# Kernel optimization log

Hardware: AMD Instinct MI355X
Metric: run time of the kernel (lower is better)

The kernel has to match this reference:

```python
import jax, jax.numpy as jnp
import numpy as np

E = 64          # num_experts
D_IN = 512      # in_features
D_OUT = 512     # out_features
T = 262144      # total routed token-slots (grouped by expert, balanced)


def setup_inputs() -> dict:
    key = jax.random.key(0)
    k1, k2 = jax.random.split(key)
    STD = 0.02
    return {
        "input": jax.random.normal(k1, (T, D_IN), dtype=jnp.float32),
        # tokens are pre-grouped by expert; balanced routing -> equal counts
        "num_experts_per_token": jnp.full((E,), T // E, dtype=jnp.int64),
        "weight": jax.random.normal(k2, (E, D_OUT, D_IN), dtype=jnp.float32) * STD,
        "bias": jnp.zeros((E, D_OUT), dtype=jnp.float32),
    }


def reference(input, num_experts_per_token, weight, bias):
    # Faithful to the split + per-expert F.linear + cat path, for balanced
    # routing (equal counts per expert) so shapes are static under jit.
    e = weight.shape[0]
    tpe = input.shape[0] // e  # tokens per expert
    x = input.reshape(e, tpe, -1)                      # [E, tpe, D_in]
    # F.linear(x_e, W_e) = x_e @ W_e.T for each expert -> grouped GEMM
    out = jnp.einsum('eti,eoi->eto', x, weight)        # [E, tpe, D_out]
    out = out + bias[:, None, :]
    return out.reshape(e * tpe, -1)                    # [T, D_out]
```

## Files before the change

### kernel.cpp

```cpp
#include <hip/hip_runtime.h>
#include <hip/hip_bf16.h>


#define NEXPERT 64
#define DIN 512
#define DOUT 512
#define TPE 4096
#define BM 256
#define BN 256
#define BK 64
#define NKT 8

typedef __attribute__((ext_vector_type(8))) __bf16 bf16x8;
typedef __attribute__((ext_vector_type(4))) float f32x4;

__global__ __launch_bounds__(256)
void pack_w_kernel(const float* __restrict__ w, __bf16* __restrict__ wp) {
  int S = blockIdx.x * 256 + threadIdx.x;
  int l  = S & 63;
  int j  = (S >> 6) & 31;
  int kt = (S >> 11) & 7;
  int nt = (S >> 14) & 1;
  int e  = S >> 15;
  int o  = nt * 256 + j * 8 + (l >> 3);
  int kc = (l & 7) ^ (l >> 3);
  const float* src = w + ((size_t)(e * DOUT + o)) * DIN + kt * BK + kc * 8;
  f32x4 lo = *(const f32x4*)(src);
  f32x4 hi = *(const f32x4*)(src + 4);
  bf16x8 r;
  r[0]=(__bf16)lo[0]; r[1]=(__bf16)lo[1]; r[2]=(__bf16)lo[2]; r[3]=(__bf16)lo[3];
  r[4]=(__bf16)hi[0]; r[5]=(__bf16)hi[1]; r[6]=(__bf16)hi[2]; r[7]=(__bf16)hi[3];
  *(bf16x8*)(wp + (size_t)S * 8) = r;
}

__global__ __launch_bounds__(512, 2)
void moe_gemm256(const float* __restrict__ x, const __bf16* __restrict__ wp,
                 const float* __restrict__ bias, float* __restrict__ out) {
  __shared__ __align__(16) unsigned char sA[2][BM * BK * 2];
  __shared__ __align__(16) unsigned char sB[2][BN * BK * 2];

  int bid  = blockIdx.x;
  int swzb = (bid & 7) * 256 + (bid >> 3);
  int e  = swzb >> 5;
  int rr = swzb & 31;
  int mt = rr >> 1;
  int nt = rr & 1;

  const int tid  = threadIdx.x;
  const int lane = tid & 63;
  const int wv   = tid >> 6;
  const int wm   = wv >> 2;
  const int wn   = wv & 3;
  const int r15  = lane & 15;
  const int kg   = lane >> 4;

  const int xt0 = ((kg)     ^ (r15 & 7)) << 4;
  const int xt1 = ((4 + kg) ^ (r15 & 7)) << 4;
  const int aRdBase = (wm * 128 + r15) * 128;
  const int bRdBase = (wn * 64  + r15) * 128;

  const int ar = tid >> 1;
  const int h  = tid & 1;
  const float* aG = x + ((size_t)e * TPE + (size_t)mt * BM + ar) * DIN + h * 32;
  const int awr0 = ar * 128;

  const __bf16* bS0 = wp + (size_t)(e * 2 + nt) * 131072
                         + (size_t)(wv * 4) * 512 + (size_t)lane * 8;

  f32x4 sa[8];

#define GLOADB(kt, dbuf)                                                     \
  { _Pragma("unroll") for (int i = 0; i < 4; ++i)                            \
      __builtin_amdgcn_global_load_lds(                                      \
          (const __attribute__((address_space(1))) void*)(bS0 +              \
              (size_t)(kt) * 16384 + i * 512),                               \
          (__attribute__((address_space(3))) void*)(&sB[dbuf][(wv * 4 + i) * 1024]), \
          16, 0, 0); }

#define ISSUEA(kt)                                                           \
  { _Pragma("unroll") for (int i = 0; i < 8; ++i)                            \
      sa[i] = *(const f32x4*)(aG + (kt) * BK + i * 4); }

#define WRITEA(dbuf)                                                         \
  { _Pragma("unroll") for (int i2 = 0; i2 < 4; ++i2) {                       \
      bf16x8 cc;                                                             \
      cc[0]=(__bf16)sa[i2*2][0];   cc[1]=(__bf16)sa[i2*2][1];                \
      cc[2]=(__bf16)sa[i2*2][2];   cc[3]=(__bf16)sa[i2*2][3];                \
      cc[4]=(__bf16)sa[i2*2+1][0]; cc[5]=(__bf16)sa[i2*2+1][1];              \
      cc[6]=(__bf16)sa[i2*2+1][2]; cc[7]=(__bf16)sa[i2*2+1][3];              \
      *(bf16x8*)(&sA[dbuf][awr0 + (((h*4+i2) ^ (ar & 7)) << 4)]) = cc; } }

#define READB(d)                                                             \
  { _Pragma("unroll") for (int ni = 0; ni < 4; ++ni) {                       \
      bfr[ni][0] = *(const bf16x8*)(&sB[d][bRdBase + ni*2048 + xt0]);        \
      bfr[ni][1] = *(const bf16x8*)(&sB[d][bRdBase + ni*2048 + xt1]); } }

#define READA(p, d, af)                                                      \
  { _Pragma("unroll") for (int mi = 0; mi < 2; ++mi) {                       \
      af[mi][0] = *(const bf16x8*)(&sA[d][aRdBase + (p)*4096 + mi*2048 + xt0]); \
      af[mi][1] = *(const bf16x8*)(&sA[d][aRdBase + (p)*4096 + mi*2048 + xt1]); } }

#define MFMAP(p, af)                                                         \
  { __builtin_amdgcn_s_setprio(1);                                           \
    _Pragma("unroll") for (int mi = 0; mi < 2; ++mi)                         \
      _Pragma("unroll") for (int ni = 0; ni < 4; ++ni)                       \
        _Pragma("unroll") for (int kk = 0; kk < 2; ++kk)                     \
          acc[(p)*2+mi][ni] = __builtin_amdgcn_mfma_f32_16x16x32_bf16(       \
              af[mi][kk], bfr[ni][kk], acc[(p)*2+mi][ni], 0, 0, 0);          \
    __builtin_amdgcn_s_setprio(0); }

  f32x4 acc[8][4];
#pragma unroll
  for (int m = 0; m < 8; ++m)
#pragma unroll
    for (int n = 0; n < 4; ++n) acc[m][n] = (f32x4)0.f;

  GLOADB(0, 0);
  ISSUEA(0);
  WRITEA(0);
  asm volatile("s_waitcnt lgkmcnt(0)" ::: "memory");
  __builtin_amdgcn_s_barrier();

  bf16x8 bfr[4][2];

#pragma unroll
  for (int t = 0; t < NKT - 1; ++t) {
    const int d = t & 1;
    GLOADB(t + 1, d ^ 1);
    ISSUEA(t + 1);
    READB(d);
    bf16x8 af0[2][2], af1[2][2], af2[2][2], af3[2][2];
    READA(0, d, af0);
    MFMAP(0, af0);
    READA(1, d, af1);
    MFMAP(1, af1);
    READA(2, d, af2);
    MFMAP(2, af2);
    READA(3, d, af3);
    WRITEA(d ^ 1);
    MFMAP(3, af3);
    asm volatile("s_waitcnt lgkmcnt(0)" ::: "memory");
    __builtin_amdgcn_s_barrier();
  }

  {
    const int d = 1;
    READB(d);
    bf16x8 af[2][2];
    READA(0, d, af); MFMAP(0, af);
    READA(1, d, af); MFMAP(1, af);
    READA(2, d, af); MFMAP(2, af);
    READA(3, d, af); MFMAP(3, af);
  }

  float bv[4];
  const float* bp = bias + (size_t)e * DOUT + nt * BN + wn * 64 + r15;
#pragma unroll
  for (int n = 0; n < 4; ++n) bv[n] = bp[n * 16];

  const int q4 = (lane >> 4) * 4;
  float* Cb = out + ((size_t)e * TPE + (size_t)mt * BM + wm * 128) * DOUT
              + nt * BN + wn * 64;
#pragma unroll
  for (int m = 0; m < 8; ++m) {
#pragma unroll
    for (int j = 0; j < 4; ++j) {
      float* pr = Cb + (size_t)(m * 16 + q4 + j) * DOUT;
#pragma unroll
      for (int n = 0; n < 4; ++n)
        pr[n * 16 + r15] = acc[m][n][j] + bv[n];
    }
  }
#undef GLOADB
#undef ISSUEA
#undef WRITEA
#undef READB
#undef READA
#undef MFMAP
}

__device__ __forceinline__ bf16x8 cvt8f(f32x4 lo, f32x4 hi) {
  bf16x8 r;
  r[0]=(__bf16)lo[0]; r[1]=(__bf16)lo[1]; r[2]=(__bf16)lo[2]; r[3]=(__bf16)lo[3];
  r[4]=(__bf16)hi[0]; r[5]=(__bf16)hi[1]; r[6]=(__bf16)hi[2]; r[7]=(__bf16)hi[3];
  return r;
}

__global__ __launch_bounds__(256)
void moe_fallback(const float* __restrict__ x, const float* __restrict__ w,
                  const float* __restrict__ bias, float* __restrict__ out) {
  __shared__ bf16x8 fA[2][512];
  __shared__ bf16x8 fB[2][512];
  int bid = blockIdx.x;
  int swz = (bid & 7) * 1024 + (bid >> 3);
  int e = swz >> 7, rr = swz & 127, mt = rr >> 2, nt = rr & 3;
  const int t = threadIdx.x, lane = t & 63, wave = t >> 6;
  const int wm = wave >> 1, wnn = wave & 1, r15 = lane & 15, kgf = lane >> 4;
  const int rs = r15 * 4 + (kgf ^ ((r15 >> 1) & 3));
  const int row0 = t >> 2, kg0 = t & 3;
  const int slot0 = row0 * 4 + (kg0 ^ ((row0 >> 1) & 3));
  const int slot1 = slot0 + 256;
  const float* Ab = x + ((size_t)e * TPE + (size_t)mt * 128) * DIN;
  const float* Bb = w + ((size_t)e * DOUT + (size_t)nt * 128) * DIN;
  const int offA0 = row0 * DIN + kg0 * 8, offA1 = offA0 + 64 * DIN;
  f32x4 a0l, a0h, a1l, a1h, b0l, b0h, b1l, b1h;
  auto LOAD = [&](int kt) {
    const float* pa0 = Ab + offA0 + kt * 32; const float* pa1 = Ab + offA1 + kt * 32;
    const float* pb0 = Bb + offA0 + kt * 32; const float* pb1 = Bb + offA1 + kt * 32;
    a0l = *(const f32x4*)(pa0); a0h = *(const f32x4*)(pa0 + 4);
    a1l = *(const f32x4*)(pa1); a1h = *(const f32x4*)(pa1 + 4);
    b0l = *(const f32x4*)(pb0); b0h = *(const f32x4*)(pb0 + 4);
    b1l = *(const f32x4*)(pb1); b1h = *(const f32x4*)(pb1 + 4);
  };
  auto STORE = [&](int buf) {
    fA[buf][slot0] = cvt8f(a0l, a0h); fA[buf][slot1] = cvt8f(a1l, a1h);
    fB[buf][slot0] = cvt8f(b0l, b0h); fB[buf][slot1] = cvt8f(b1l, b1h);
  };
  f32x4 acc[4][4];
#pragma unroll
  for (int m = 0; m < 4; ++m)
#pragma unroll
    for (int n = 0; n < 4; ++n) acc[m][n] = (f32x4)0.f;
  LOAD(0); STORE(0); __syncthreads();
  int cur = 0;
  for (int kt = 0; kt < 16; ++kt) {
    if (kt + 1 < 16) LOAD(kt + 1);
    bf16x8 af[4], bfr[4];
#pragma unroll
    for (int m = 0; m < 4; ++m) af[m] = fA[cur][wm * 256 + m * 64 + rs];
#pragma unroll
    for (int n = 0; n < 4; ++n) bfr[n] = fB[cur][wnn * 256 + n * 64 + rs];
#pragma unroll
    for (int m = 0; m < 4; ++m)
#pragma unroll
      for (int n = 0; n < 4; ++n)
        acc[m][n] = __builtin_amdgcn_mfma_f32_16x16x32_bf16(af[m], bfr[n], acc[m][n], 0, 0, 0);
    if (kt + 1 < 16) { STORE(cur ^ 1); __syncthreads(); }
    cur ^= 1;
  }
  float bv[4];
  const float* bp = bias + (size_t)e * DOUT + nt * 128 + wnn * 64 + r15;
#pragma unroll
  for (int n = 0; n < 4; ++n) bv[n] = bp[n * 16];
  const int q4 = (lane >> 4) * 4;
  float* Cb = out + ((size_t)e * TPE + (size_t)mt * 128 + wm * 64) * DOUT + nt * 128 + wnn * 64;
#pragma unroll
  for (int m = 0; m < 4; ++m)
#pragma unroll
    for (int j = 0; j < 4; ++j) {
      float* pr = Cb + (size_t)(m * 16 + q4 + j) * DOUT;
#pragma unroll
      for (int n = 0; n < 4; ++n) pr[n * 16 + r15] = acc[m][n][j] + bv[n];
    }
}

extern "C" void kernel_launch(void* const* d_in, const int* in_sizes, int n_in,
                              void* d_out, int out_size, void* d_ws, size_t ws_size,
                              hipStream_t stream) {
  const float* x    = (const float*)d_in[0];
  const float* w    = (const float*)d_in[2];
  const float* bias = (const float*)d_in[3];
  float* out        = (float*)d_out;

  const size_t wElems = (size_t)NEXPERT * DOUT * DIN;
  const size_t needWs = wElems * sizeof(__hip_bfloat16);

  if (ws_size >= needWs) {
    dim3 pgrid(wElems / 8 / 256);
    hipLaunchKernelGGL(pack_w_kernel, pgrid, dim3(256), 0, stream,
                       w, (__bf16*)d_ws);
    dim3 grid(NEXPERT * (TPE / BM) * (DOUT / BN));
    hipLaunchKernelGGL(moe_gemm256, grid, dim3(512), 0, stream,
                       x, (const __bf16*)d_ws, bias, out);
  } else {
    dim3 grid(NEXPERT * 32 * 4);
    hipLaunchKernelGGL(moe_fallback, grid, dim3(256), 0, stream, x, w, bias, out);
  }
}
```

Measured before the change: 355.1 us.

## Restructure K-loop into barrier-synchronized phases with staggered loads

Rewrites the main K loop into four phases per tile, each ending in a workgroup barrier plus an LDS wait before its MFMA block. The global B load now starts after phase 0 and the A register writes wait on explicit vmcnt counts, so memory ops interleave with compute in lockstep across waves. The peeled last iteration is folded into the loop through a stage flag. This adds many extra barriers per tile, which could stall waves that would otherwise overlap freely.

```diff
diff --git a/kernel.cpp b/kernel.cpp
--- a/kernel.cpp
+++ b/kernel.cpp
@@ -100,6 +100,11 @@
       af[mi][0] = *(const bf16x8*)(&sA[d][aRdBase + (p)*4096 + mi*2048 + xt0]); \
       af[mi][1] = *(const bf16x8*)(&sA[d][aRdBase + (p)*4096 + mi*2048 + xt1]); } }
 
+#define PHASE_SYNC_IN()                                                      \
+  { __builtin_amdgcn_s_barrier();                                            \
+    asm volatile("s_waitcnt lgkmcnt(0)" ::: "memory");                       \
+    __builtin_amdgcn_sched_barrier(0); }
+
 #define MFMAP(p, af)                                                         \
   { __builtin_amdgcn_s_setprio(1);                                           \
     _Pragma("unroll") for (int mi = 0; mi < 2; ++mi)                         \
@@ -121,36 +126,45 @@
   asm volatile("s_waitcnt lgkmcnt(0)" ::: "memory");
   __builtin_amdgcn_s_barrier();
 
-  bf16x8 bfr[4][2];
-
-#pragma unroll
-  for (int t = 0; t < NKT - 1; ++t) {
+#pragma unroll
+  for (int t = 0; t < NKT; ++t) {
     const int d = t & 1;
-    GLOADB(t + 1, d ^ 1);
-    ISSUEA(t + 1);
+    const bool stage = (t + 1 < NKT);
+    bf16x8 bfr[4][2];
+
+    if (stage) ISSUEA(t + 1);
     READB(d);
-    bf16x8 af0[2][2], af1[2][2], af2[2][2], af3[2][2];
+    bf16x8 af0[2][2];
     READA(0, d, af0);
+    PHASE_SYNC_IN();
     MFMAP(0, af0);
+    __builtin_amdgcn_s_barrier();
+
+    if (stage) GLOADB(t + 1, d ^ 1);
+    bf16x8 af1[2][2];
     READA(1, d, af1);
+    PHASE_SYNC_IN();
     MFMAP(1, af1);
+    __builtin_amdgcn_s_barrier();
+
+    bf16x8 af2[2][2];
     READA(2, d, af2);
+    PHASE_SYNC_IN();
     MFMAP(2, af2);
+    __builtin_amdgcn_s_barrier();
+
+    bf16x8 af3[2][2];
     READA(3, d, af3);
-    WRITEA(d ^ 1);
+    if (stage) {
+      asm volatile("s_waitcnt vmcnt(4)" ::: "memory");
+      WRITEA(d ^ 1);
+    }
+    PHASE_SYNC_IN();
     MFMAP(3, af3);
-    asm volatile("s_waitcnt lgkmcnt(0)" ::: "memory");
-    __builtin_amdgcn_s_barrier();
-  }
-
-  {
-    const int d = 1;
-    READB(d);
-    bf16x8 af[2][2];
-    READA(0, d, af); MFMAP(0, af);
-    READA(1, d, af); MFMAP(1, af);
-    READA(2, d, af); MFMAP(2, af);
-    READA(3, d, af); MFMAP(3, af);
+    if (stage) {
+      asm volatile("s_waitcnt vmcnt(0)" ::: "memory");
+    }
+    __builtin_amdgcn_s_barrier();
   }
 
   float bv[4];
@@ -176,6 +190,7 @@
 #undef WRITEA
 #undef READB
 #undef READA
+#undef PHASE_SYNC_IN
 #undef MFMAP
 }
 
```

New measurement: 353.6 us. Within noise of the previous version (-0.4%).
